# Optimization experiments

Hardware: AMD Instinct MI355X
Metric: run time of the kernel (lower is better)

Reference implementation:

```python
import jax, jax.numpy as jnp
import numpy as np

N_HEAD = 16
N_EMBD = 1024
SPARSE_BLOCK = 64  # band width: keys j with i-64 <= j <= i are visible
B, T = 2, 2048


def setup_inputs() -> dict:
    key = jax.random.key(0)
    ks = jax.random.split(key, 5)
    C = N_EMBD
    scale = 0.02
    return {
        "x": jax.random.normal(ks[0], (B, T, C), dtype=jnp.float32),
        "Wqkv": jax.random.normal(ks[1], (C, 3 * C), dtype=jnp.float32) * scale,
        "bqkv": jnp.zeros((3 * C,), dtype=jnp.float32),
        "Wproj": jax.random.normal(ks[2], (C, C), dtype=jnp.float32) * scale,
        "bproj": jnp.zeros((C,), dtype=jnp.float32),
    }


def reference(x, Wqkv, bqkv, Wproj, bproj):
    Bz, Tz, C = x.shape
    H, D = N_HEAD, C // N_HEAD
    qkv = x @ Wqkv + bqkv                       # [B,T,3C]
    q, k, v = jnp.split(qkv, 3, axis=-1)

    def heads(t):  # [B,T,C] -> [B,H,T,D]
        return t.reshape(Bz, Tz, H, D).transpose(0, 2, 1, 3)
    q, k, v = heads(q), heads(k), heads(v)

    scale = 1.0 / jnp.sqrt(jnp.float32(D))
    att = jnp.einsum("bhtd,bhsd->bhts", q, k) * scale  # [B,H,T,T]

    # causal + local band mask: key j visible to query i iff i-64 <= j <= i
    i = jnp.arange(Tz)[:, None]
    j = jnp.arange(Tz)[None, :]
    mask = (j <= i) & (j >= i - SPARSE_BLOCK)           # [T,T] bool
    att = jnp.where(mask[None, None], att, -jnp.inf)
    att = jax.nn.softmax(att, axis=-1)

    y = jnp.einsum("bhts,bhsd->bhtd", att, v)           # [B,H,T,D]
    y = y.transpose(0, 2, 1, 3).reshape(Bz, Tz, C)
    return y @ Wproj + bproj
```

## Files before the change

### kernel.cpp

```cpp
#include <hip/hip_runtime.h>
#include <hip/hip_bf16.h>
#include <math.h>

#define N_HEAD 16
#define N_EMBD 1024
#define HEADD  64
#define BANDW  64
#define BB     2
#define TT     2048

typedef __attribute__((ext_vector_type(8))) short bf16x8;
typedef __attribute__((ext_vector_type(4))) float f32x4;

__device__ __forceinline__ ushort f2b(float f) {
    __hip_bfloat16 h = __float2bfloat16(f);
    union { __hip_bfloat16 h; ushort u; } cv; cv.h = h; return cv.u;
}
__device__ __forceinline__ float b2f(ushort u) { return __uint_as_float(((unsigned)u) << 16); }

#define GLOAD16(gp, lp) \
    __builtin_amdgcn_global_load_lds((const __attribute__((address_space(1))) void*)(gp), \
                                     (__attribute__((address_space(3))) void*)(lp), 16, 0, 0)

__global__ __launch_bounds__(256) void k_prep(
    const float* __restrict__ Wqkv, ushort* __restrict__ wqkvT,
    const float* __restrict__ Wproj, ushort* __restrict__ wprojT)
{
    __shared__ float tile[32][33];
    int bid = blockIdx.x;
    int t = threadIdx.x;
    const float* in; ushort* out; int R, C, bx, by;
    if (bid < 3072) {
        in = Wqkv; out = wqkvT; R = 1024; C = 3072;
        bx = bid % 96; by = bid / 96;
    } else {
        int b3 = bid - 3072;
        in = Wproj; out = wprojT; R = 1024; C = 1024;
        bx = b3 & 31; by = b3 >> 5;
    }
    int tx = t & 31, ty = t >> 5;
    int c0 = bx * 32, r0 = by * 32;
    for (int rr = ty; rr < 32; rr += 8)
        tile[rr][tx] = in[(size_t)(r0 + rr) * C + (c0 + tx)];
    __syncthreads();
    for (int cc = ty; cc < 32; cc += 8)
        out[(size_t)(c0 + cc) * R + (r0 + tx)] = f2b(tile[tx][cc]);
}

#define CVT8(CV, FA, FB) do { \
    CV[0] = (short)f2b(FA[0]); CV[1] = (short)f2b(FA[1]); \
    CV[2] = (short)f2b(FA[2]); CV[3] = (short)f2b(FA[3]); \
    CV[4] = (short)f2b(FB[0]); CV[5] = (short)f2b(FB[1]); \
    CV[6] = (short)f2b(FB[2]); CV[7] = (short)f2b(FB[3]); \
} while (0)

template <bool OUT_BF16>
__global__ __launch_bounds__(512, 4) void k_gemm1(
    const float* __restrict__ Xf, const ushort* __restrict__ BT,
    const float* __restrict__ bias, void* __restrict__ Cout,
    int M, int N, int K)
{
    __shared__ __align__(16) char lds[2 * 32768];
    const int K2 = K * 2;
    int t = threadIdx.x, lane = t & 63, w = t >> 6;
    int wm = w >> 2, wn = w & 3;
    int lr = lane & 15, kg = lane >> 4;

    int nbx = N >> 7;
    int cpx = gridDim.x >> 3;
    int wg = blockIdx.x;
    int wgid = (wg & 7) * cpx + (wg >> 3);
    int bx = wgid % nbx, by = wgid / nbx;
    int row0 = by * 128, col0 = bx * 128;

    unsigned voffA0, voffA1;
    int oA0 = w * 2048 + lane * 16, oA1 = oA0 + 1024;
    {
        int r0 = oA0 >> 7, c0 = ((oA0 >> 4) - r0) & 7;
        voffA0 = (unsigned)((row0 + r0) * (K * 4) + c0 * 32);
        int r1 = oA1 >> 7, c1 = ((oA1 >> 4) - r1) & 7;
        voffA1 = (unsigned)((row0 + r1) * (K * 4) + c1 * 32);
    }
    unsigned long xs = (unsigned long)Xf;

    size_t sB0, sB1;
    {
        int o = w * 2048 + lane * 16;
        int r = o >> 7, c = ((o >> 4) - r) & 7;
        sB0 = (size_t)r * K2 + c * 16;
        o += 1024; r = o >> 7; c = ((o >> 4) - r) & 7;
        sB1 = (size_t)r * K2 + c * 16;
    }
    const char* gB = (const char*)BT + (size_t)col0 * K2;

    int offA[4][2], offB[2][2];
#pragma unroll
    for (int m = 0; m < 4; ++m) {
        int rr = wm * 64 + m * 16 + lr;
#pragma unroll
        for (int ks = 0; ks < 2; ++ks)
            offA[m][ks] = rr * 128 + (((ks * 4 + kg) + rr) & 7) * 16;
    }
#pragma unroll
    for (int n = 0; n < 2; ++n) {
        int rr = wn * 32 + n * 16 + lr;
#pragma unroll
        for (int ks = 0; ks < 2; ++ks)
            offB[n][ks] = 16384 + rr * 128 + (((ks * 4 + kg) + rr) & 7) * 16;
    }

    f32x4 acc[4][2];
#pragma unroll
    for (int i = 0; i < 4; ++i)
#pragma unroll
        for (int j = 0; j < 2; ++j) { f32x4 z = {0.f, 0.f, 0.f, 0.f}; acc[i][j] = z; }

#define LOADA(TI, F0, F1, F2, F3) do { \
        unsigned _v0 = voffA0 + (unsigned)(TI) * 256u; \
        unsigned _v1 = voffA1 + (unsigned)(TI) * 256u; \
        asm volatile("global_load_dwordx4 %0, %1, %2"           : "=v"(F0) : "v"(_v0), "s"(xs) : "memory"); \
        asm volatile("global_load_dwordx4 %0, %1, %2 offset:16" : "=v"(F1) : "v"(_v0), "s"(xs) : "memory"); \
        asm volatile("global_load_dwordx4 %0, %1, %2"           : "=v"(F2) : "v"(_v1), "s"(xs) : "memory"); \
        asm volatile("global_load_dwordx4 %0, %1, %2 offset:16" : "=v"(F3) : "v"(_v1), "s"(xs) : "memory"); \
    } while (0)
#define STGB(BUF, TI) do { \
        char* _db = lds + (BUF) * 32768 + 16384; \
        const char* _gb = gB + (size_t)(TI) * 128; \
        GLOAD16(_gb + sB0, _db + w * 2048); \
        GLOAD16(_gb + sB1, _db + w * 2048 + 1024); \
    } while (0)

    int nt = K >> 6;
    {
        f32x4 p0, p1, p2, p3, p4, p5, p6, p7;
        LOADA(0, p0, p1, p2, p3);
        STGB(0, 0);
        LOADA(1, p4, p5, p6, p7);
        STGB(1, 1);
        asm volatile("s_waitcnt vmcnt(2)" ::: "memory");
        __builtin_amdgcn_sched_barrier(0);
        bf16x8 c0, c1;
        CVT8(c0, p0, p1); CVT8(c1, p2, p3);
        *(bf16x8*)(lds + oA0) = c0;
        *(bf16x8*)(lds + oA1) = c1;
        CVT8(c0, p4, p5); CVT8(c1, p6, p7);
        *(bf16x8*)(lds + 32768 + oA0) = c0;
        *(bf16x8*)(lds + 32768 + oA1) = c1;
        asm volatile("s_waitcnt lgkmcnt(0)" ::: "memory");
        __builtin_amdgcn_s_barrier();
    }

#pragma unroll 2
    for (int tt = 0; tt < nt; ++tt) {
        int cur = tt & 1;
        char* bufb = lds + cur * 32768;
        bf16x8 af[4][2], bfr[2][2];
#pragma unroll
        for (int ks = 0; ks < 2; ++ks) {
#pragma unroll
            for (int m = 0; m < 4; ++m)
                af[m][ks] = *(const bf16x8*)(bufb + offA[m][ks]);
#pragma unroll
            for (int n = 0; n < 2; ++n)
                bfr[n][ks] = *(const bf16x8*)(bufb + offB[n][ks]);
        }
        asm volatile("s_waitcnt lgkmcnt(0)" ::: "memory");
        __builtin_amdgcn_sched_barrier(0);
        __builtin_amdgcn_s_barrier();
        bool st = (tt + 2 < nt);
        f32x4 q0, q1, q2, q3;
        if (st) {
            LOADA(tt + 2, q0, q1, q2, q3);
            STGB(cur, tt + 2);
        }
#pragma unroll
        for (int ks = 0; ks < 2; ++ks)
#pragma unroll
            for (int m = 0; m < 4; ++m)
#pragma unroll
                for (int n = 0; n < 2; ++n)
                    acc[m][n] = __builtin_amdgcn_mfma_f32_16x16x32_bf16(
                        af[m][ks], bfr[n][ks], acc[m][n], 0, 0, 0);
        if (st)
            asm volatile("s_waitcnt vmcnt(2)" ::: "memory");
        else
            asm volatile("s_waitcnt vmcnt(0)" ::: "memory");
        __builtin_amdgcn_sched_barrier(0);
        if (st) {
            bf16x8 c0, c1;
            CVT8(c0, q0, q1); CVT8(c1, q2, q3);
            *(bf16x8*)(bufb + oA0) = c0;
            *(bf16x8*)(bufb + oA1) = c1;
        }
        asm volatile("s_waitcnt lgkmcnt(0)" ::: "memory");
        __builtin_amdgcn_s_barrier();
    }
#undef LOADA
#undef STGB

#pragma unroll
    for (int m = 0; m < 4; ++m) {
        int growb = row0 + wm * 64 + m * 16 + kg * 4;
#pragma unroll
        for (int n = 0; n < 2; ++n) {
            int gcol = col0 + wn * 32 + n * 16 + lr;
            float bv = bias ? bias[gcol] : 0.f;
#pragma unroll
            for (int e = 0; e < 4; ++e) {
                float val = acc[m][n][e] + bv;
                if (OUT_BF16)
                    ((ushort*)Cout)[(size_t)(growb + e) * N + gcol] = f2b(val);
                else
                    ((float*)Cout)[(size_t)(growb + e) * N + gcol] = val;
            }
        }
    }
}

template <bool OUT_BF16>
__global__ __launch_bounds__(256, 3) void k_gemm2(
    const ushort* __restrict__ A, const ushort* __restrict__ BT,
    const float* __restrict__ bias, void* __restrict__ Cout,
    int M, int N, int K)
{
    __shared__ __align__(16) char lds[2 * 24576];
    const int K2 = K * 2;
    int t = threadIdx.x, lane = t & 63, w = t >> 6;
    int wm = w >> 1, wn = w & 1;
    int lr = lane & 15, kg = lane >> 4;

    int nbx = N >> 6;
    int cpx = gridDim.x >> 3;
    int wg = blockIdx.x;
    int wgid = (wg & 7) * cpx + (wg >> 3);
    int bx = wgid % nbx, by = wgid / nbx;
    int row0 = by * 128, col0 = bx * 64;

    size_t sA[4], sB[2];
#pragma unroll
    for (int u = 0; u < 4; ++u) {
        int o = w * 4096 + u * 1024 + lane * 16;
        int r = o >> 7, c = ((o >> 4) - r) & 7;
        sA[u] = (size_t)r * K2 + c * 16;
    }
#pragma unroll
    for (int u = 0; u < 2; ++u) {
        int o = w * 2048 + u * 1024 + lane * 16;
        int r = o >> 7, c = ((o >> 4) - r) & 7;
        sB[u] = (size_t)r * K2 + c * 16;
    }
    const char* gA = (const char*)A  + (size_t)row0 * K2;
    const char* gB = (const char*)BT + (size_t)col0 * K2;

    int offA[4][2], offB[2][2];
#pragma unroll
    for (int m = 0; m < 4; ++m) {
        int rr = wm * 64 + m * 16 + lr;
#pragma unroll
        for (int ks = 0; ks < 2; ++ks)
            offA[m][ks] = rr * 128 + (((ks * 4 + kg) + rr) & 7) * 16;
    }
#pragma unroll
    for (int n = 0; n < 2; ++n) {
        int rr = wn * 32 + n * 16 + lr;
#pragma unroll
        for (int ks = 0; ks < 2; ++ks)
            offB[n][ks] = rr * 128 + (((ks * 4 + kg) + rr) & 7) * 16;
    }

    f32x4 acc[4][2];
#pragma unroll
    for (int i = 0; i < 4; ++i)
#pragma unroll
        for (int j = 0; j < 2; ++j) { f32x4 z = {0.f, 0.f, 0.f, 0.f}; acc[i][j] = z; }

#define STAGE2(BUF, TI) do { \
        char* _db = lds + (BUF) * 24576; \
        const char* _ga = gA + (size_t)(TI) * 128; \
        const char* _gb = gB + (size_t)(TI) * 128; \
        GLOAD16(_ga + sA[0], _db + w * 4096); \
        GLOAD16(_ga + sA[1], _db + w * 4096 + 1024); \
        GLOAD16(_ga + sA[2], _db + w * 4096 + 2048); \
        GLOAD16(_ga + sA[3], _db + w * 4096 + 3072); \
        GLOAD16(_gb + sB[0], _db + 16384 + w * 2048); \
        GLOAD16(_gb + sB[1], _db + 16384 + w * 2048 + 1024); \
    } while (0)

    int nt = K >> 6;
    STAGE2(0, 0);
    STAGE2(1, 1);
    asm volatile("s_waitcnt vmcnt(6)" ::: "memory");
    __builtin_amdgcn_s_barrier();

#pragma unroll 2
    for (int tt = 0; tt < nt; ++tt) {
        int cur = tt & 1;
        const char* bufb = lds + cur * 24576;
        bf16x8 af[4][2], bfr[2][2];
#pragma unroll
        for (int ks = 0; ks < 2; ++ks) {
#pragma unroll
            for (int m = 0; m < 4; ++m)
                af[m][ks] = *(const bf16x8*)(bufb + offA[m][ks]);
#pragma unroll
            for (int n = 0; n < 2; ++n)
                bfr[n][ks] = *(const bf16x8*)(bufb + 16384 + offB[n][ks]);
        }
        asm volatile("s_waitcnt lgkmcnt(0)" ::: "memory");
        __builtin_amdgcn_sched_barrier(0);
        __builtin_amdgcn_s_barrier();
        if (tt + 2 < nt) STAGE2(cur, tt + 2);
#pragma unroll
        for (int ks = 0; ks < 2; ++ks)
#pragma unroll
            for (int m = 0; m < 4; ++m)
#pragma unroll
                for (int n = 0; n < 2; ++n)
                    acc[m][n] = __builtin_amdgcn_mfma_f32_16x16x32_bf16(
                        af[m][ks], bfr[n][ks], acc[m][n], 0, 0, 0);
        if (tt + 2 < nt)
            asm volatile("s_waitcnt vmcnt(6)" ::: "memory");
        else
            asm volatile("s_waitcnt vmcnt(0)" ::: "memory");
        __builtin_amdgcn_s_barrier();
    }
#undef STAGE2

#pragma unroll
    for (int m = 0; m < 4; ++m) {
        int growb = row0 + wm * 64 + m * 16 + kg * 4;
#pragma unroll
        for (int n = 0; n < 2; ++n) {
            int gcol = col0 + wn * 32 + n * 16 + lr;
            float bv = bias ? bias[gcol] : 0.f;
#pragma unroll
            for (int e = 0; e < 4; ++e) {
                float val = acc[m][n][e] + bv;
                if (OUT_BF16)
                    ((ushort*)Cout)[(size_t)(growb + e) * N + gcol] = f2b(val);
                else
                    ((float*)Cout)[(size_t)(growb + e) * N + gcol] = val;
            }
        }
    }
}

__global__ __launch_bounds__(256) void k_attn(const ushort* __restrict__ qkv,
                                              ushort* __restrict__ y) {
    __shared__ __align__(16) ushort Ks[128 * 64];
    __shared__ ushort Vt[64][136];
    __shared__ ushort Ps[64][136];

    const int R3 = 3 * N_EMBD;
    int bid = blockIdx.x;
    int l  = (bid & 7) * 128 + (bid >> 3);
    int qt = l & 31;
    int h  = (l >> 5) & (N_HEAD - 1);
    int b  = l >> 9;
    int i0 = qt * 64;
    int j0 = i0 - BANDW;
    int hc = h * HEADD;

    int t    = threadIdx.x;
    int lane = t & 63;
    int wq   = t >> 6;
    int lr   = lane & 15;
    int kg   = lane >> 4;

    const ushort* kbase_g = qkv + (size_t)b * TT * R3 + N_EMBD + hc;
#pragma unroll
    for (int rnd = 0; rnd < 4; ++rnd) {
        int o = wq * 4096 + rnd * 1024 + lane * 16;
        int row  = o >> 7;
        int cblk = (((o >> 4) & 7) - row) & 7;
        int j = j0 + row; if (j < 0) j = 0;
        GLOAD16((const char*)(kbase_g + (size_t)j * R3) + cblk * 16,
                (char*)Ks + wq * 4096 + rnd * 1024);
    }

    {
        int row  = t >> 1;
        int part = t & 1;
        int j = j0 + row;
        if (j >= 0) {
            const ushort* vrow = qkv + (size_t)(b * TT + j) * R3 + 2 * N_EMBD + hc + part * 32;
#pragma unroll
            for (int c = 0; c < 4; ++c) {
                uint4 vv = reinterpret_cast<const uint4*>(vrow)[c];
                const ushort* pv = (const ushort*)&vv;
                int dbase = part * 32 + c * 8;
#pragma unroll
                for (int e = 0; e < 8; ++e)
                    Vt[dbase + e][row] = pv[e];
            }
        } else {
#pragma unroll
            for (int c = 0; c < 4; ++c) {
                int dbase = part * 32 + c * 8;
#pragma unroll
                for (int e = 0; e < 8; ++e)
                    Vt[dbase + e][row] = 0;
            }
        }
    }

    const ushort* qbase = qkv + (size_t)(b * TT + i0 + wq * 16 + lr) * R3 + hc;
    bf16x8 aq0 = *reinterpret_cast<const bf16x8*>(qbase + kg * 8);
    bf16x8 aq1 = *reinterpret_cast<const bf16x8*>(qbase + 32 + kg * 8);

    __syncthreads();

    f32x4 s[8];
#pragma unroll
    for (int nt = 0; nt < 8; ++nt) { f32x4 z = {0.f, 0.f, 0.f, 0.f}; s[nt] = z; }
#pragma unroll
    for (int nt = 0; nt < 8; ++nt) {
        int row = nt * 16 + lr;
        const char* kr = (const char*)Ks + row * 128;
        bf16x8 kb0 = *(const bf16x8*)(kr + (((kg)     + row) & 7) * 16);
        bf16x8 kb1 = *(const bf16x8*)(kr + (((4 + kg) + row) & 7) * 16);
        s[nt] = __builtin_amdgcn_mfma_f32_16x16x32_bf16(aq0, kb0, s[nt], 0, 0, 0);
        s[nt] = __builtin_amdgcn_mfma_f32_16x16x32_bf16(aq1, kb1, s[nt], 0, 0, 0);
    }

    float mx[4] = {-INFINITY, -INFINITY, -INFINITY, -INFINITY};
#pragma unroll
    for (int nt = 0; nt < 8; ++nt) {
        int kc = nt * 16 + lr;
#pragma unroll
        for (int e = 0; e < 4; ++e) {
            int qr = wq * 16 + kg * 4 + e;
            bool valid = (kc >= qr) && (kc <= qr + BANDW) && (j0 + kc >= 0);
            float v = s[nt][e] * 0.125f;
            s[nt][e] = valid ? v : -INFINITY;
            mx[e] = fmaxf(mx[e], s[nt][e]);
        }
    }
#pragma unroll
    for (int e = 0; e < 4; ++e) {
#pragma unroll
        for (int m = 1; m <= 8; m <<= 1)
            mx[e] = fmaxf(mx[e], __shfl_xor(mx[e], m, 64));
    }
    float sm[4] = {0.f, 0.f, 0.f, 0.f};
#pragma unroll
    for (int nt = 0; nt < 8; ++nt) {
        int kc = nt * 16 + lr;
#pragma unroll
        for (int e = 0; e < 4; ++e) {
            float p = __expf(s[nt][e] - mx[e]);
            sm[e] += p;
            Ps[wq * 16 + kg * 4 + e][kc] = f2b(p);
        }
    }
#pragma unroll
    for (int e = 0; e < 4; ++e) {
#pragma unroll
        for (int m = 1; m <= 8; m <<= 1)
            sm[e] += __shfl_xor(sm[e], m, 64);
    }

    f32x4 o[4];
#pragma unroll
    for (int vt = 0; vt < 4; ++vt) { f32x4 z = {0.f, 0.f, 0.f, 0.f}; o[vt] = z; }
#pragma unroll
    for (int ks = 0; ks < 4; ++ks) {
        bf16x8 pa = *reinterpret_cast<const bf16x8*>(&Ps[wq * 16 + lr][ks * 32 + kg * 8]);
#pragma unroll
        for (int vt = 0; vt < 4; ++vt) {
            bf16x8 vb = *reinterpret_cast<const bf16x8*>(&Vt[vt * 16 + lr][ks * 32 + kg * 8]);
            o[vt] = __builtin_amdgcn_mfma_f32_16x16x32_bf16(pa, vb, o[vt], 0, 0, 0);
        }
    }

    float inv[4];
#pragma unroll
    for (int e = 0; e < 4; ++e) inv[e] = 1.f / sm[e];

#pragma unroll
    for (int vt = 0; vt < 4; ++vt) {
#pragma unroll
        for (int e = 0; e < 4; ++e) {
            int qr = wq * 16 + kg * 4 + e;
            y[(size_t)(b * TT + i0 + qr) * N_EMBD + hc + vt * 16 + lr] =
                f2b(o[vt][e] * inv[e]);
        }
    }
}

extern "C" void kernel_launch(void* const* d_in, const int* in_sizes, int n_in,
                              void* d_out, int out_size, void* d_ws, size_t ws_size,
                              hipStream_t stream) {
    const float* x     = (const float*)d_in[0];
    const float* Wqkv  = (const float*)d_in[1];
    const float* bqkv  = (const float*)d_in[2];
    const float* Wproj = (const float*)d_in[3];
    const float* bproj = (const float*)d_in[4];
    float* out = (float*)d_out;

    const int M  = BB * TT;
    const int C  = N_EMBD;
    const int N1 = 3 * C;

    char* ws = (char*)d_ws;
    ushort* wqkvT  = (ushort*)ws; ws += (size_t)N1 * C * 2;
    ushort* wprojT = (ushort*)ws; ws += (size_t)C  * C * 2;
    ushort* qkvb   = (ushort*)ws; ws += (size_t)M  * N1 * 2;
    ushort* yb     = (ushort*)ws; ws += (size_t)M  * C * 2;

    k_prep<<<4096, 256, 0, stream>>>(Wqkv, wqkvT, Wproj, wprojT);
    {
        int nwg = (M / 128) * (N1 / 128);
        k_gemm1<true><<<nwg, 512, 0, stream>>>(x, wqkvT, bqkv, (void*)qkvb, M, N1, C);
    }
    k_attn<<<BB * N_HEAD * (TT / 64), 256, 0, stream>>>(qkvb, yb);
    {
        int nwg = (M / 128) * (C / 64);
        k_gemm2<false><<<nwg, 256, 0, stream>>>(yb, wprojT, bproj, (void*)out, M, C, C);
    }
}
```

Before: 82.69 us.

## Deepen A-operand register prefetch in GEMM1 to overlap fp32 loads across two tiles

Replaces the inline-asm fp32 A loads with plain vector pointer loads and keeps two register buffers of A data in flight. The bf16 conversion and LDS store for the next tile now happen right after the MFMAs, using data loaded one iteration earlier, instead of waiting for the loads issued in the same iteration. The goal is to hide global-load latency for the A operand behind more compute. In exchange it uses more VGPRs, which at launch bounds of 4 waves per SIMD may cause spills, and the vmcnt counts rely on the compiler emitting loads in the expected order.

```diff
diff --git a/kernel.cpp b/kernel.cpp
--- a/kernel.cpp
+++ b/kernel.cpp
@@ -73,15 +73,14 @@
     int bx = wgid % nbx, by = wgid / nbx;
     int row0 = by * 128, col0 = bx * 128;
 
-    unsigned voffA0, voffA1;
     int oA0 = w * 2048 + lane * 16, oA1 = oA0 + 1024;
+    const char* gxA0; const char* gxA1;
     {
         int r0 = oA0 >> 7, c0 = ((oA0 >> 4) - r0) & 7;
-        voffA0 = (unsigned)((row0 + r0) * (K * 4) + c0 * 32);
+        gxA0 = (const char*)Xf + (size_t)(row0 + r0) * (K * 4) + c0 * 32;
         int r1 = oA1 >> 7, c1 = ((oA1 >> 4) - r1) & 7;
-        voffA1 = (unsigned)((row0 + r1) * (K * 4) + c1 * 32);
-    }
-    unsigned long xs = (unsigned long)Xf;
+        gxA1 = (const char*)Xf + (size_t)(row0 + r1) * (K * 4) + c1 * 32;
+    }
 
     size_t sB0, sB1;
     {
@@ -115,13 +114,10 @@
 #pragma unroll
         for (int j = 0; j < 2; ++j) { f32x4 z = {0.f, 0.f, 0.f, 0.f}; acc[i][j] = z; }
 
-#define LOADA(TI, F0, F1, F2, F3) do { \
-        unsigned _v0 = voffA0 + (unsigned)(TI) * 256u; \
-        unsigned _v1 = voffA1 + (unsigned)(TI) * 256u; \
-        asm volatile("global_load_dwordx4 %0, %1, %2"           : "=v"(F0) : "v"(_v0), "s"(xs) : "memory"); \
-        asm volatile("global_load_dwordx4 %0, %1, %2 offset:16" : "=v"(F1) : "v"(_v0), "s"(xs) : "memory"); \
-        asm volatile("global_load_dwordx4 %0, %1, %2"           : "=v"(F2) : "v"(_v1), "s"(xs) : "memory"); \
-        asm volatile("global_load_dwordx4 %0, %1, %2 offset:16" : "=v"(F3) : "v"(_v1), "s"(xs) : "memory"); \
+#define LOADA_P(TI, D) do { \
+        const f32x4* _p0 = (const f32x4*)(gxA0 + (size_t)(TI) * 256); \
+        const f32x4* _p1 = (const f32x4*)(gxA1 + (size_t)(TI) * 256); \
+        D[0] = _p0[0]; D[1] = _p0[1]; D[2] = _p1[0]; D[3] = _p1[1]; \
     } while (0)
 #define STGB(BUF, TI) do { \
         char* _db = lds + (BUF) * 32768 + 16384; \
@@ -131,29 +127,31 @@
     } while (0)
 
     int nt = K >> 6;
+    f32x4 arA[2][4];
     {
-        f32x4 p0, p1, p2, p3, p4, p5, p6, p7;
-        LOADA(0, p0, p1, p2, p3);
+        f32x4 p[4];
+        LOADA_P(0, p);
+        __builtin_amdgcn_sched_barrier(0);
         STGB(0, 0);
-        LOADA(1, p4, p5, p6, p7);
+        __builtin_amdgcn_sched_barrier(0);
+        LOADA_P(1, arA[1]);
+        __builtin_amdgcn_sched_barrier(0);
         STGB(1, 1);
-        asm volatile("s_waitcnt vmcnt(2)" ::: "memory");
         __builtin_amdgcn_sched_barrier(0);
         bf16x8 c0, c1;
-        CVT8(c0, p0, p1); CVT8(c1, p2, p3);
+        CVT8(c0, p[0], p[1]); CVT8(c1, p[2], p[3]);
         *(bf16x8*)(lds + oA0) = c0;
         *(bf16x8*)(lds + oA1) = c1;
-        CVT8(c0, p4, p5); CVT8(c1, p6, p7);
-        *(bf16x8*)(lds + 32768 + oA0) = c0;
-        *(bf16x8*)(lds + 32768 + oA1) = c1;
+        asm volatile("s_waitcnt vmcnt(6)" ::: "memory");
         asm volatile("s_waitcnt lgkmcnt(0)" ::: "memory");
         __builtin_amdgcn_s_barrier();
     }
 
 #pragma unroll 2
     for (int tt = 0; tt < nt; ++tt) {
-        int cur = tt & 1;
+        const int cur = tt & 1;
         char* bufb = lds + cur * 32768;
+        char* bufo = lds + (cur ^ 1) * 32768;
         bf16x8 af[4][2], bfr[2][2];
 #pragma unroll
         for (int ks = 0; ks < 2; ++ks) {
@@ -168,10 +166,12 @@
         __builtin_amdgcn_sched_barrier(0);
         __builtin_amdgcn_s_barrier();
         bool st = (tt + 2 < nt);
-        f32x4 q0, q1, q2, q3;
+        bool cv = (tt + 1 < nt);
         if (st) {
-            LOADA(tt + 2, q0, q1, q2, q3);
+            LOADA_P(tt + 2, arA[cur]);
+            __builtin_amdgcn_sched_barrier(0);
             STGB(cur, tt + 2);
+            __builtin_amdgcn_sched_barrier(0);
         }
 #pragma unroll
         for (int ks = 0; ks < 2; ++ks)
@@ -181,21 +181,22 @@
                 for (int n = 0; n < 2; ++n)
                     acc[m][n] = __builtin_amdgcn_mfma_f32_16x16x32_bf16(
                         af[m][ks], bfr[n][ks], acc[m][n], 0, 0, 0);
+        __builtin_amdgcn_sched_barrier(0);
+        if (cv) {
+            bf16x8 c0, c1;
+            CVT8(c0, arA[cur ^ 1][0], arA[cur ^ 1][1]);
+            CVT8(c1, arA[cur ^ 1][2], arA[cur ^ 1][3]);
+            *(bf16x8*)(bufo + oA0) = c0;
+            *(bf16x8*)(bufo + oA1) = c1;
+        }
         if (st)
-            asm volatile("s_waitcnt vmcnt(2)" ::: "memory");
+            asm volatile("s_waitcnt vmcnt(6)" ::: "memory");
         else
             asm volatile("s_waitcnt vmcnt(0)" ::: "memory");
-        __builtin_amdgcn_sched_barrier(0);
-        if (st) {
-            bf16x8 c0, c1;
-            CVT8(c0, q0, q1); CVT8(c1, q2, q3);
-            *(bf16x8*)(bufb + oA0) = c0;
-            *(bf16x8*)(bufb + oA1) = c1;
-        }
         asm volatile("s_waitcnt lgkmcnt(0)" ::: "memory");
         __builtin_amdgcn_s_barrier();
     }
-#undef LOADA
+#undef LOADA_P
 #undef STGB
 
 #pragma unroll
```

Result: slower. 124.0 us (+50.0%).
